# Kernel tuning notes

Hardware: AMD Instinct MI355X
Metric: run time of the kernel (lower is better)

## Reference

```python
import jax, jax.numpy as jnp
import numpy as np

NNZ_PER_ROW = 204


def setup_inputs() -> dict:
    key = jax.random.key(0)
    k1, k2, k3, k4, k5 = jax.random.split(key, 5)
    O, I = 4096, 4096
    x = jax.random.normal(k1, (4, 2048, I), dtype=jnp.float32)
    # packed int4 pairs: each byte holds two offset-int4 values in [0, 16)
    base_packed = jax.random.randint(k2, (O, I // 2), 0, 256, dtype=jnp.int32)
    # per-output-row dequant scale (ceiling/7 > 0)
    scales = jax.random.uniform(k3, (O,), dtype=jnp.float32, minval=0.001, maxval=0.05)
    nnz = O * NNZ_PER_ROW
    ortho_vals = jax.random.normal(k4, (nnz,), dtype=jnp.float32) * 0.01
    ortho_indices = jax.random.randint(k5, (nnz,), 0, I, dtype=jnp.int32)
    ortho_ptr = (jnp.arange(O + 1, dtype=jnp.int32) * NNZ_PER_ROW)
    return {"x": x, "base_packed": base_packed, "scales": scales,
            "ortho_vals": ortho_vals, "ortho_indices": ortho_indices,
            "ortho_ptr": ortho_ptr}


def reference(x, base_packed, scales, ortho_vals, ortho_indices, ortho_ptr):
    O, half = base_packed.shape
    I = 2 * half
    alpha = 1.0
    # --- unpack int4: low nibble -> even cols, high nibble -> odd cols ---
    low = base_packed & 0xF          # [O, I/2]
    high = base_packed >> 4          # [O, I/2]
    q = jnp.stack([low, high], axis=-1).reshape(O, I) - 8  # signed int4 in [-8, 7]
    w_base = q.astype(jnp.float32) * scales[:, None]       # dequant [O, I]
    # --- CSR sparse residual -> dense (reference form of fused CSR add) ---
    nnz = ortho_vals.shape[0]
    rows = jnp.searchsorted(ortho_ptr, jnp.arange(nnz, dtype=jnp.int32), side='right') - 1
    w_sparse = jnp.zeros((O, I), jnp.float32).at[rows, ortho_indices].add(
        ortho_vals.astype(jnp.float32))
    # --- fused matmul: out = x @ (W_base + alpha * W_sparse)^T ---
    w = w_base + alpha * w_sparse
    x_flat = x.reshape(-1, I).astype(jnp.float32)
    out = x_flat @ w.T                                     # [tokens, O]
    return out.reshape(x.shape[:-1] + (O,)).astype(x.dtype)
```

## Files before the change

kernel.cpp:

```cpp
#include <hip/hip_runtime.h>
#include <stdint.h>

#define O_DIM 4096
#define I_DIM 4096
#define BM 128
#define BN 128
#define BK 32

typedef short bf16x8 __attribute__((ext_vector_type(8)));
typedef float f32x4 __attribute__((ext_vector_type(4)));
typedef int i32x4 __attribute__((ext_vector_type(4)));
typedef unsigned short u16;
typedef u16 u16x4 __attribute__((ext_vector_type(4)));
typedef u16 u16x8 __attribute__((ext_vector_type(8)));

__device__ __forceinline__ u16 f2bf(float f) {
  uint32_t u = __builtin_bit_cast(uint32_t, f);
  u += 0x7FFFu + ((u >> 16) & 1u);
  return (u16)(u >> 16);
}

#define GLOAD_LDS16(gsrc, ldst)                                                   \
  __builtin_amdgcn_global_load_lds(                                               \
      (const __attribute__((address_space(1))) uint32_t*)(gsrc),                  \
      (__attribute__((address_space(3))) uint32_t*)(ldst), 16, 0, 0)

__global__ __launch_bounds__(256) void prep_w(
    const int* __restrict__ packed, const float* __restrict__ scales,
    const float* __restrict__ vals, const int* __restrict__ idx,
    const int* __restrict__ ptr, u16* __restrict__ Whi) {
  __shared__ float row[I_DIM];
  int o = blockIdx.x;
  float s = scales[o];
  const i32x4* prow = (const i32x4*)(packed + (size_t)o * (I_DIM / 2));
  for (int i = threadIdx.x; i < I_DIM / 8; i += 256) {
    i32x4 v = prow[i];
#pragma unroll
    for (int c = 0; c < 4; ++c) {
      int pv = v[c];
      row[8 * i + 2 * c]     = (float)((pv & 0xF) - 8) * s;
      row[8 * i + 2 * c + 1] = (float)(((pv >> 4) & 0xF) - 8) * s;
    }
  }
  __syncthreads();
  int b = ptr[o], e = ptr[o + 1];
  for (int j = b + (int)threadIdx.x; j < e; j += 256)
    atomicAdd(&row[idx[j]], vals[j]);
  __syncthreads();
  size_t base = (size_t)o * I_DIM;
  for (int i = threadIdx.x; i < I_DIM / 8; i += 256) {
    u16x8 hv;
#pragma unroll
    for (int c = 0; c < 8; ++c) hv[c] = f2bf(row[8 * i + c]);
    *(u16x8*)&Whi[base + 8 * i] = hv;
  }
}

__global__ __launch_bounds__(256) void prep_x(
    const float* __restrict__ x, u16* __restrict__ Xhi, int n8) {
  int i = blockIdx.x * 256 + threadIdx.x;
  int stride = gridDim.x * 256;
  for (; i < n8; i += stride) {
    f32x4 v0 = ((const f32x4*)x)[2 * i];
    f32x4 v1 = ((const f32x4*)x)[2 * i + 1];
    u16x8 h;
#pragma unroll
    for (int c = 0; c < 4; ++c) {
      h[c]     = f2bf(v0[c]);
      h[c + 4] = f2bf(v1[c]);
    }
    ((u16x8*)Xhi)[i] = h;
  }
}

__global__ __launch_bounds__(256, 2) void gemm1(
    const u16* __restrict__ Xhi, const u16* __restrict__ Whi,
    float* __restrict__ out, int mtiles) {
  __shared__ u16 Ah[BM * BK];
  __shared__ u16 Bh[BN * BK];

  int ntiles = O_DIM / BN;
  int nwg = mtiles * ntiles;
  int per = nwg >> 3;
  int bid = blockIdx.x;
  int swz = (bid & 7) * per + (bid >> 3);
  int tm = swz % mtiles;
  int tn = swz / mtiles;
  int m0 = tm * BM, n0 = tn * BN;

  int t = threadIdx.x;
  int lane = t & 63;
  int wave = t >> 6;
  int wr = wave >> 1, wc = wave & 1;
  int l15 = lane & 15, lhi = lane >> 4;

  int srow = t >> 2;
  int sk8 = (t & 3) * 8;
  const u16* asrc = Xhi + (size_t)(m0 + srow) * I_DIM + sk8;
  const u16* bsrc = Whi + (size_t)(n0 + srow) * I_DIM + sk8;
  u16* adst = Ah + (size_t)(t & ~63) * 8;
  u16* bdst = Bh + (size_t)(t & ~63) * 8;

  f32x4 acc[4][4];
#pragma unroll
  for (int m = 0; m < 4; ++m)
#pragma unroll
    for (int n = 0; n < 4; ++n) acc[m][n] = (f32x4)0.0f;

  const bf16x8* A8 = (const bf16x8*)Ah;
  const bf16x8* B8 = (const bf16x8*)Bh;

  for (int k0 = 0; k0 < I_DIM; k0 += BK) {
    GLOAD_LDS16(asrc + k0, adst);
    GLOAD_LDS16(asrc + (size_t)64 * I_DIM + k0, adst + 64 * BK);
    GLOAD_LDS16(bsrc + k0, bdst);
    GLOAD_LDS16(bsrc + (size_t)64 * I_DIM + k0, bdst + 64 * BK);
    __syncthreads();

    bf16x8 fa[4], fb[4];
#pragma unroll
    for (int m = 0; m < 4; ++m) {
      int r = wr * 64 + m * 16 + l15;
      fa[m] = A8[r * 4 + lhi];
    }
#pragma unroll
    for (int n = 0; n < 4; ++n) {
      int r = wc * 64 + n * 16 + l15;
      fb[n] = B8[r * 4 + lhi];
    }

#pragma unroll
    for (int m = 0; m < 4; ++m)
#pragma unroll
      for (int n = 0; n < 4; ++n)
        acc[m][n] = __builtin_amdgcn_mfma_f32_16x16x32_bf16(fa[m], fb[n], acc[m][n], 0, 0, 0);
    __syncthreads();
  }

#pragma unroll
  for (int m = 0; m < 4; ++m) {
    int row = m0 + wr * 64 + m * 16 + lhi * 4;
#pragma unroll
    for (int n = 0; n < 4; ++n) {
      int col = n0 + wc * 64 + n * 16 + l15;
      float* op = out + (size_t)row * O_DIM + col;
#pragma unroll
      for (int r = 0; r < 4; ++r)
        op[(size_t)r * O_DIM] = acc[m][n][r];
    }
  }
}

extern "C" void kernel_launch(void* const* d_in, const int* in_sizes, int n_in,
                              void* d_out, int out_size, void* d_ws, size_t ws_size,
                              hipStream_t stream) {
  const float* x      = (const float*)d_in[0];
  const int* packed   = (const int*)d_in[1];
  const float* scales = (const float*)d_in[2];
  const float* vals   = (const float*)d_in[3];
  const int* idx      = (const int*)d_in[4];
  const int* ptr      = (const int*)d_in[5];
  float* out          = (float*)d_out;

  int nx = in_sizes[0];
  int tokens = nx / I_DIM;
  int mtiles = tokens / BM;
  int nwg = mtiles * (O_DIM / BN);

  u16* Whi = (u16*)d_ws;
  u16* Xhi = Whi + (size_t)O_DIM * I_DIM;

  prep_w<<<O_DIM, 256, 0, stream>>>(packed, scales, vals, idx, ptr, Whi);
  prep_x<<<2048, 256, 0, stream>>>(x, Xhi, nx / 8);
  gemm1<<<nwg, 256, 0, stream>>>(Xhi, Whi, out, mtiles);
}
```

Baseline: 617.4 us.

## Replace GEMM with 256x256 tile, 8-wave pipelined kernel on pre-swizzled panels

The weight and activation prep kernels now write bf16 data in a panelized, XOR-swizzled layout so each K-tile is a contiguous block that loads straight into LDS without bank conflicts. The GEMM becomes a 512-thread, 256x256-tile kernel with a double-buffered 128KB dynamic LDS ping-pong. It interleaves global-to-LDS loads with MFMA phases, using explicit barriers, s_setprio and vmcnt waits. The aim is more data reuse per tile and hiding memory latency behind compute, at the cost of hardcoded shapes and heavy register use.

```diff
diff --git a/kernel.cpp b/kernel.cpp
--- a/kernel.cpp
+++ b/kernel.cpp
@@ -3,15 +3,14 @@
 
 #define O_DIM 4096
 #define I_DIM 4096
-#define BM 128
-#define BN 128
-#define BK 32
+#define TOKENS 8192
+#define NKT 64
+#define PANEL_U16 16384
 
 typedef short bf16x8 __attribute__((ext_vector_type(8)));
 typedef float f32x4 __attribute__((ext_vector_type(4)));
 typedef int i32x4 __attribute__((ext_vector_type(4)));
 typedef unsigned short u16;
-typedef u16 u16x4 __attribute__((ext_vector_type(4)));
 typedef u16 u16x8 __attribute__((ext_vector_type(8)));
 
 __device__ __forceinline__ u16 f2bf(float f) {
@@ -28,7 +27,7 @@
 __global__ __launch_bounds__(256) void prep_w(
     const int* __restrict__ packed, const float* __restrict__ scales,
     const float* __restrict__ vals, const int* __restrict__ idx,
-    const int* __restrict__ ptr, u16* __restrict__ Whi) {
+    const int* __restrict__ ptr, u16* __restrict__ Wp) {
   __shared__ float row[I_DIM];
   int o = blockIdx.x;
   float s = scales[o];
@@ -47,108 +46,153 @@
   for (int j = b + (int)threadIdx.x; j < e; j += 256)
     atomicAdd(&row[idx[j]], vals[j]);
   __syncthreads();
-  size_t base = (size_t)o * I_DIM;
-  for (int i = threadIdx.x; i < I_DIM / 8; i += 256) {
-    u16x8 hv;
-#pragma unroll
-    for (int c = 0; c < 8; ++c) hv[c] = f2bf(row[8 * i + c]);
-    *(u16x8*)&Whi[base + 8 * i] = hv;
+  int cb = o >> 8, r = o & 255, rx = r & 7;
+  for (int c16g = threadIdx.x; c16g < 512; c16g += 256) {
+    u16x8 h;
+#pragma unroll
+    for (int c = 0; c < 8; ++c) h[c] = f2bf(row[c16g * 8 + c]);
+    int kt = c16g >> 3, c16 = c16g & 7;
+    size_t chunk = (size_t)(cb * NKT + kt) * 2048 + r * 8 + (c16 ^ rx);
+    *(u16x8*)(Wp + chunk * 8) = h;
   }
 }
 
 __global__ __launch_bounds__(256) void prep_x(
-    const float* __restrict__ x, u16* __restrict__ Xhi, int n8) {
-  int i = blockIdx.x * 256 + threadIdx.x;
+    const float* __restrict__ x, u16* __restrict__ Xp, int nchunks) {
+  int g = blockIdx.x * 256 + threadIdx.x;
   int stride = gridDim.x * 256;
-  for (; i < n8; i += stride) {
-    f32x4 v0 = ((const f32x4*)x)[2 * i];
-    f32x4 v1 = ((const f32x4*)x)[2 * i + 1];
+  for (; g < nchunks; g += stride) {
+    int rowg = g >> 9;
+    int c16g = g & 511;
+    const float* s = x + ((size_t)rowg << 12) + (c16g << 3);
+    f32x4 v0 = *(const f32x4*)s;
+    f32x4 v1 = *(const f32x4*)(s + 4);
     u16x8 h;
 #pragma unroll
-    for (int c = 0; c < 4; ++c) {
-      h[c]     = f2bf(v0[c]);
-      h[c + 4] = f2bf(v1[c]);
+    for (int c = 0; c < 4; ++c) { h[c] = f2bf(v0[c]); h[c + 4] = f2bf(v1[c]); }
+    int rb = rowg >> 8, r = rowg & 255, kt = c16g >> 3, c16 = c16g & 7;
+    size_t chunk = (size_t)(rb * NKT + kt) * 2048 + r * 8 + (c16 ^ (r & 7));
+    *(u16x8*)(Xp + chunk * 8) = h;
+  }
+}
+
+#define BAR()   asm volatile("s_barrier" ::: "memory")
+#define SCHEDB() __builtin_amdgcn_sched_barrier(0)
+#define PRIO1() __builtin_amdgcn_s_setprio(1)
+#define PRIO0() __builtin_amdgcn_s_setprio(0)
+#define VMW4()  asm volatile("s_waitcnt vmcnt(4)" ::: "memory")
+#define VMW0()  asm volatile("s_waitcnt vmcnt(0)" ::: "memory")
+
+#define STG_A(bb, kt, j) GLOAD_LDS16(Apan + (kt)*PANEL_U16 + (j)*4096 + stSrc, \
+                                     lds + (bb)*32768 + (j)*4096 + stDst)
+#define STG_B(bb, kt, j) GLOAD_LDS16(Bpan + (kt)*PANEL_U16 + (j)*4096 + stSrc, \
+                                     lds + (bb)*32768 + 16384 + (j)*4096 + stDst)
+#define SA0(bb, kt) { STG_A(bb, kt, 0); STG_A(bb, kt, 1); }
+#define SA1(bb, kt) { STG_A(bb, kt, 2); STG_A(bb, kt, 3); }
+#define SB0(bb, kt) { STG_B(bb, kt, 0); STG_B(bb, kt, 1); }
+#define SB1(bb, kt) { STG_B(bb, kt, 2); STG_B(bb, kt, 3); }
+
+#define RD_A(bb, MB) { const bf16x8* P = (const bf16x8*)lds + (bb)*4096;       \
+  _Pragma("unroll") for (int fm = 0; fm < 4; ++fm) {                           \
+    a[fm][0] = P[aBase + (MB + fm) * 128 + x0];                                \
+    a[fm][1] = P[aBase + (MB + fm) * 128 + x1]; } }
+#define RD_B(bb, FNB) { const bf16x8* P = (const bf16x8*)lds + (bb)*4096 + 2048;\
+  _Pragma("unroll") for (int fn = 0; fn < 2; ++fn) {                           \
+    b[FNB + fn][0] = P[bBase + (FNB + fn) * 128 + x0];                         \
+    b[FNB + fn][1] = P[bBase + (FNB + fn) * 128 + x1]; } }
+
+#define MMQ(MB, FNB)                                                           \
+  _Pragma("unroll") for (int fm = 0; fm < 4; ++fm)                             \
+  _Pragma("unroll") for (int fn = 0; fn < 2; ++fn) {                           \
+    acc[MB+fm][FNB+fn] = __builtin_amdgcn_mfma_f32_16x16x32_bf16(              \
+        a[fm][0], b[FNB+fn][0], acc[MB+fm][FNB+fn], 0, 0, 0);                  \
+    acc[MB+fm][FNB+fn] = __builtin_amdgcn_mfma_f32_16x16x32_bf16(              \
+        a[fm][1], b[FNB+fn][1], acc[MB+fm][FNB+fn], 0, 0, 0); }
+
+#define MFMA_PHASE(MB, FNB) { BAR(); PRIO1(); MMQ(MB, FNB); PRIO0(); BAR(); }
+
+__global__ __launch_bounds__(512, 2) void gemm8p(
+    const u16* __restrict__ Xp, const u16* __restrict__ Wp,
+    float* __restrict__ out) {
+  extern __shared__ u16 lds[];
+
+  int bid = blockIdx.x;
+  int swz = (bid & 7) * 64 + (bid >> 3);
+  int tm = swz & 31;
+  int tn = swz >> 5;
+  const u16* Apan = Xp + (size_t)tm * (NKT * PANEL_U16);
+  const u16* Bpan = Wp + (size_t)tn * (NKT * PANEL_U16);
+
+  int t = threadIdx.x;
+  int lane = t & 63, wid = t >> 6;
+  int wm = wid >> 2, wn = wid & 3;
+  int l15 = lane & 15, lhi = lane >> 4;
+  int x0 = lhi ^ (l15 & 7);
+  int x1 = (4 + lhi) ^ (l15 & 7);
+  int aBase = (wm * 128 + l15) * 8;
+  int bBase = (wn * 64 + l15) * 8;
+  int stSrc = t * 8;
+  int stDst = (t & ~63) * 8;
+
+  f32x4 acc[8][4];
+#pragma unroll
+  for (int m = 0; m < 8; ++m)
+#pragma unroll
+    for (int n = 0; n < 4; ++n) acc[m][n] = (f32x4)0.0f;
+  bf16x8 a[4][2], b[4][2];
+
+  SA0(0, 0); SA1(0, 0); SB0(0, 0); SB1(0, 0);
+  SB0(1, 1); SB1(1, 1);
+  VMW4(); BAR(); SCHEDB();
+
+#pragma unroll 1
+  for (int i = 0; i < 31; ++i) {
+    int kt0 = 2 * i;
+    RD_A(0, 0); RD_B(0, 0); SA0(1, kt0 + 1);
+    MFMA_PHASE(0, 0);
+    RD_B(0, 2); SA1(1, kt0 + 1);
+    MFMA_PHASE(0, 2);
+    RD_A(0, 4); SB0(0, kt0 + 2);
+    MFMA_PHASE(4, 0);
+    SB1(0, kt0 + 2); VMW4();
+    MFMA_PHASE(4, 2); SCHEDB();
+    RD_A(1, 0); RD_B(1, 0); SA0(0, kt0 + 2);
+    MFMA_PHASE(0, 0);
+    RD_B(1, 2); SA1(0, kt0 + 2);
+    MFMA_PHASE(0, 2);
+    RD_A(1, 4); SB0(1, kt0 + 3);
+    MFMA_PHASE(4, 0);
+    SB1(1, kt0 + 3); VMW4();
+    MFMA_PHASE(4, 2); SCHEDB();
+  }
+
+  RD_A(0, 0); RD_B(0, 0); SA0(1, 63);
+  MFMA_PHASE(0, 0);
+  RD_B(0, 2); SA1(1, 63);
+  MFMA_PHASE(0, 2);
+  RD_A(0, 4);
+  MFMA_PHASE(4, 0);
+  VMW0();
+  MFMA_PHASE(4, 2); SCHEDB();
+  RD_A(1, 0); RD_B(1, 0);
+  MFMA_PHASE(0, 0);
+  RD_B(1, 2);
+  MFMA_PHASE(0, 2);
+  RD_A(1, 4);
+  MFMA_PHASE(4, 0);
+  PRIO1(); MMQ(4, 2); PRIO0();
+
+  int orow = tm * 256 + wm * 128 + lhi * 4;
+  int ocol = tn * 256 + wn * 64 + l15;
+#pragma unroll
+  for (int fm = 0; fm < 8; ++fm)
+#pragma unroll
+    for (int fn = 0; fn < 4; ++fn) {
+      float* op = out + (size_t)(orow + fm * 16) * O_DIM + ocol + fn * 16;
+#pragma unroll
+      for (int r = 0; r < 4; ++r)
+        op[(size_t)r * O_DIM] = acc[fm][fn][r];
     }
-    ((u16x8*)Xhi)[i] = h;
-  }
-}
-
-__global__ __launch_bounds__(256, 2) void gemm1(
-    const u16* __restrict__ Xhi, const u16* __restrict__ Whi,
-    float* __restrict__ out, int mtiles) {
-  __shared__ u16 Ah[BM * BK];
-  __shared__ u16 Bh[BN * BK];
-
-  int ntiles = O_DIM / BN;
-  int nwg = mtiles * ntiles;
-  int per = nwg >> 3;
-  int bid = blockIdx.x;
-  int swz = (bid & 7) * per + (bid >> 3);
-  int tm = swz % mtiles;
-  int tn = swz / mtiles;
-  int m0 = tm * BM, n0 = tn * BN;
-
-  int t = threadIdx.x;
-  int lane = t & 63;
-  int wave = t >> 6;
-  int wr = wave >> 1, wc = wave & 1;
-  int l15 = lane & 15, lhi = lane >> 4;
-
-  int srow = t >> 2;
-  int sk8 = (t & 3) * 8;
-  const u16* asrc = Xhi + (size_t)(m0 + srow) * I_DIM + sk8;
-  const u16* bsrc = Whi + (size_t)(n0 + srow) * I_DIM + sk8;
-  u16* adst = Ah + (size_t)(t & ~63) * 8;
-  u16* bdst = Bh + (size_t)(t & ~63) * 8;
-
-  f32x4 acc[4][4];
-#pragma unroll
-  for (int m = 0; m < 4; ++m)
-#pragma unroll
-    for (int n = 0; n < 4; ++n) acc[m][n] = (f32x4)0.0f;
-
-  const bf16x8* A8 = (const bf16x8*)Ah;
-  const bf16x8* B8 = (const bf16x8*)Bh;
-
-  for (int k0 = 0; k0 < I_DIM; k0 += BK) {
-    GLOAD_LDS16(asrc + k0, adst);
-    GLOAD_LDS16(asrc + (size_t)64 * I_DIM + k0, adst + 64 * BK);
-    GLOAD_LDS16(bsrc + k0, bdst);
-    GLOAD_LDS16(bsrc + (size_t)64 * I_DIM + k0, bdst + 64 * BK);
-    __syncthreads();
-
-    bf16x8 fa[4], fb[4];
-#pragma unroll
-    for (int m = 0; m < 4; ++m) {
-      int r = wr * 64 + m * 16 + l15;
-      fa[m] = A8[r * 4 + lhi];
-    }
-#pragma unroll
-    for (int n = 0; n < 4; ++n) {
-      int r = wc * 64 + n * 16 + l15;
-      fb[n] = B8[r * 4 + lhi];
-    }
-
-#pragma unroll
-    for (int m = 0; m < 4; ++m)
-#pragma unroll
-      for (int n = 0; n < 4; ++n)
-        acc[m][n] = __builtin_amdgcn_mfma_f32_16x16x32_bf16(fa[m], fb[n], acc[m][n], 0, 0, 0);
-    __syncthreads();
-  }
-
-#pragma unroll
-  for (int m = 0; m < 4; ++m) {
-    int row = m0 + wr * 64 + m * 16 + lhi * 4;
-#pragma unroll
-    for (int n = 0; n < 4; ++n) {
-      int col = n0 + wc * 64 + n * 16 + l15;
-      float* op = out + (size_t)row * O_DIM + col;
-#pragma unroll
-      for (int r = 0; r < 4; ++r)
-        op[(size_t)r * O_DIM] = acc[m][n][r];
-    }
-  }
 }
 
 extern "C" void kernel_launch(void* const* d_in, const int* in_sizes, int n_in,
@@ -162,15 +206,13 @@
   const int* ptr      = (const int*)d_in[5];
   float* out          = (float*)d_out;
 
-  int nx = in_sizes[0];
-  int tokens = nx / I_DIM;
-  int mtiles = tokens / BM;
-  int nwg = mtiles * (O_DIM / BN);
-
-  u16* Whi = (u16*)d_ws;
-  u16* Xhi = Whi + (size_t)O_DIM * I_DIM;
-
-  prep_w<<<O_DIM, 256, 0, stream>>>(packed, scales, vals, idx, ptr, Whi);
-  prep_x<<<2048, 256, 0, stream>>>(x, Xhi, nx / 8);
-  gemm1<<<nwg, 256, 0, stream>>>(Xhi, Whi, out, mtiles);
-}
+  u16* Wp = (u16*)d_ws;
+  u16* Xp = Wp + (size_t)16 * NKT * PANEL_U16;
+
+  prep_w<<<O_DIM, 256, 0, stream>>>(packed, scales, vals, idx, ptr, Wp);
+  prep_x<<<2048, 256, 0, stream>>>(x, Xp, TOKENS * 512);
+
+  hipFuncSetAttribute((const void*)gemm8p,
+                      hipFuncAttributeMaxDynamicSharedMemorySize, 131072);
+  gemm8p<<<512, 512, 131072, stream>>>(Xp, Wp, out);
+}
```

Result: faster. 495.2 us (-19.8%).
